# Optimization experiments

Hardware: AMD Instinct MI355X
Metric: run time of the kernel (lower is better)

## Reference

```python
import jax, jax.numpy as jnp
import numpy as np

D_MODEL = 1024
N_HEADS = 16
HEAD_DIM = D_MODEL // N_HEADS
B, S = 4, 2048


def setup_inputs() -> dict:
    key = jax.random.key(0)
    ks = jax.random.split(key, 12)
    s = 1.0 / np.sqrt(D_MODEL)
    inp = {
        'query': jax.random.normal(ks[0], (B, S, D_MODEL), jnp.float32),
        'key': jax.random.normal(ks[1], (B, S, D_MODEL), jnp.float32),
        'value': jax.random.normal(ks[2], (B, S, D_MODEL), jnp.float32),
        # causal mask, broadcast over batch and heads: [1,1,S,S]
        'mask': jnp.tril(jnp.ones((S, S), jnp.int32))[None, None],
        'Wq': jax.random.normal(ks[3], (D_MODEL, D_MODEL), jnp.float32) * s,
        'bq': jnp.zeros((D_MODEL,), jnp.float32),
        'Wk': jax.random.normal(ks[4], (D_MODEL, D_MODEL), jnp.float32) * s,
        'bk': jnp.zeros((D_MODEL,), jnp.float32),
        'Wv': jax.random.normal(ks[5], (D_MODEL, D_MODEL), jnp.float32) * s,
        'bv': jnp.zeros((D_MODEL,), jnp.float32),
        'Wo': jax.random.normal(ks[6], (D_MODEL, D_MODEL), jnp.float32) * s,
        'bo': jnp.zeros((D_MODEL,), jnp.float32),
    }
    return inp


def reference(query, key, value, mask, Wq, bq, Wk, bk, Wv, bv, Wo, bo):
    b, q_len, _ = query.shape
    scale = jnp.sqrt(jnp.float32(HEAD_DIM))
    # projections
    q = query @ Wq + bq
    k = key @ Wk + bk
    v = value @ Wv + bv
    # [b, h, s, hd]
    q = q.reshape(b, q_len, N_HEADS, HEAD_DIM).transpose(0, 2, 1, 3)
    k = k.reshape(b, -1, N_HEADS, HEAD_DIM).transpose(0, 2, 1, 3)
    v = v.reshape(b, -1, N_HEADS, HEAD_DIM).transpose(0, 2, 1, 3)
    scores = jnp.einsum('bhqd,bhkd->bhqk', q, k) / scale
    scores = jnp.where(mask == 0, jnp.float32(-jnp.inf), scores)
    attn = jax.nn.softmax(scores, axis=-1)  # dropout p=0 / eval mode
    out = jnp.einsum('bhqk,bhkd->bhqd', attn, v)
    out = out.transpose(0, 2, 1, 3).reshape(b, q_len, D_MODEL)
    return out @ Wo + bo
```

## Files before the change

### kernel.cpp

```cpp
#include <hip/hip_runtime.h>
#include <hip/hip_bf16.h>

typedef __attribute__((ext_vector_type(8))) short short8;
typedef __attribute__((ext_vector_type(4))) float floatx4;
typedef __attribute__((ext_vector_type(4))) unsigned short ushort4v;

#define D_MODEL 1024
#define S_LEN   2048
#define N_HEADS 16
#define HEAD_DIM 64
#define BATCH   4

__device__ __forceinline__ unsigned short f2bf(float x) {
    union { float f; unsigned int u; } v; v.f = x;
    unsigned int u = v.u;
    unsigned int r = (u + 0x7FFFu + ((u >> 16) & 1u)) >> 16;
    return (unsigned short)r;
}
__device__ __forceinline__ unsigned short f2bf_trunc(float x) {
    union { float f; unsigned int u; } v; v.f = x;
    return (unsigned short)(v.u >> 16);
}

__device__ __forceinline__ void gload_lds16(const void* g, void* s) {
    __builtin_amdgcn_global_load_lds(
        (const __attribute__((address_space(1))) void*)g,
        (__attribute__((address_space(3))) void*)s, 16, 0, 0);
}

struct Conv3 {
    const float* src[3];
    unsigned short* dst[3];
};

__global__ __launch_bounds__(256) void conv_bf16(Conv3 a) {
    const float* s = a.src[blockIdx.z];
    unsigned short* d = a.dst[blockIdx.z];
    size_t i = ((size_t)blockIdx.x * 256 + threadIdx.x) * 8;
    float4 f0 = *(const float4*)(s + i);
    float4 f1 = *(const float4*)(s + i + 4);
    short8 v;
    v[0] = (short)f2bf(f0.x); v[1] = (short)f2bf(f0.y);
    v[2] = (short)f2bf(f0.z); v[3] = (short)f2bf(f0.w);
    v[4] = (short)f2bf(f1.x); v[5] = (short)f2bf(f1.y);
    v[6] = (short)f2bf(f1.z); v[7] = (short)f2bf(f1.w);
    *(short8*)(d + i) = v;
}

struct Trans4 {
    const float* W[4];
    unsigned short* Wt[4];
};

__global__ __launch_bounds__(256) void transpose_w(Trans4 args) {
    __shared__ unsigned short tile[32][33];
    const float* W = args.W[blockIdx.z];
    unsigned short* Wt = args.Wt[blockIdx.z];
    int n0 = blockIdx.x * 32;
    int k0 = blockIdx.y * 32;
    int t = threadIdx.x;
    int r = t >> 5, c = t & 31;
    for (int i = 0; i < 4; ++i) {
        int k = k0 + r + i * 8;
        tile[r + i * 8][c] = f2bf(W[(size_t)k * D_MODEL + n0 + c]);
    }
    __syncthreads();
    for (int i = 0; i < 4; ++i) {
        int n = n0 + r + i * 8;
        Wt[(size_t)n * D_MODEL + k0 + c] = tile[c][r + i * 8];
    }
}

struct GemmIn {
    const unsigned short* A;
    const unsigned short* Bt;
    const float* bias;
    void* C;
    int mode;
    float scale;
};
struct Gemm3 { GemmIn g[3]; };

#define BAR()   asm volatile("s_barrier" ::: "memory")
#define LGKM0() asm volatile("s_waitcnt lgkmcnt(0)" ::: "memory")
#define VMW2()  asm volatile("s_waitcnt vmcnt(2)" ::: "memory")
#define VMW0()  asm volatile("s_waitcnt vmcnt(0)" ::: "memory")

#define READ_A4(BUF)                                                           \
    _Pragma("unroll") for (int ii = 0; ii < 4; ++ii) {                         \
        aF[ii][0] = *(const short8*)&lds[(BUF)*16384 + aOff + ii*512];         \
        aF[ii][1] = *(const short8*)&lds[(BUF)*16384 + aOff + ii*512 + 4096];  \
    }
#define READ_B4(BUF)                                                           \
    _Pragma("unroll") for (int jj = 0; jj < 4; ++jj) {                         \
        bF[jj][0] = *(const short8*)&lds[(BUF)*16384 + bOff + jj*512];         \
        bF[jj][1] = *(const short8*)&lds[(BUF)*16384 + bOff + jj*512 + 4096];  \
    }
#define MFMA_ALL()                                                             \
    __builtin_amdgcn_s_setprio(1);                                             \
    _Pragma("unroll") for (int ii = 0; ii < 4; ++ii)                           \
    _Pragma("unroll") for (int jj = 0; jj < 4; ++jj) {                         \
        acc[ii][jj] = __builtin_amdgcn_mfma_f32_16x16x32_bf16(                 \
            aF[ii][0], bF[jj][0], acc[ii][jj], 0, 0, 0);                       \
        acc[ii][jj] = __builtin_amdgcn_mfma_f32_16x16x32_bf16(                 \
            aF[ii][1], bF[jj][1], acc[ii][jj], 0, 0, 0);                       \
    }                                                                          \
    __builtin_amdgcn_s_setprio(0)

__global__ __launch_bounds__(256, 2) void gemm_128(Gemm3 args) {
    constexpr int K = D_MODEL, N = D_MODEL;
    constexpr int NT = K / 64;
    GemmIn g = args.g[blockIdx.z];

    __shared__ __align__(16) unsigned short lds[32768];

    const int m0 = blockIdx.x * 128;
    const int n0 = blockIdx.y * 128;
    const int t = threadIdx.x;
    const int w = t >> 6, lane = t & 63;
    const int quad = lane >> 4, l16 = lane & 15;
    const int wm = w >> 1, wn = w & 1;

    const int srow = w * 32 + (lane >> 2);
    const int scol = ((lane & 3) * 8) ^ ((lane & 32) ? 16 : 0);

    const int fx = (quad * 8) ^ ((l16 & 8) ? 16 : 0);
    const int aOff = (wm * 64 + l16) * 32 + fx;
    const int bOff = 8192 + (wn * 64 + l16) * 32 + fx;

    floatx4 acc[4][4] = {};
    short8 aF[4][2], bF[4][2];

    auto stageA = [&](int buf, int kt) {
        const unsigned short* s0 = g.A + (size_t)(m0 + srow) * K + kt * 64 + scol;
        unsigned short* d0 = &lds[buf * 16384 + (w * 32) * 32];
        gload_lds16(s0, d0);
        gload_lds16(s0 + 32, d0 + 4096);
        gload_lds16(s0 + (size_t)16 * K, d0 + 512);
        gload_lds16(s0 + (size_t)16 * K + 32, d0 + 512 + 4096);
    };
    auto stageB = [&](int buf, int kt) {
        const unsigned short* s0 = g.Bt + (size_t)(n0 + srow) * K + kt * 64 + scol;
        unsigned short* d0 = &lds[buf * 16384 + 8192 + (w * 32) * 32];
        gload_lds16(s0, d0);
        gload_lds16(s0 + 32, d0 + 4096);
        gload_lds16(s0 + (size_t)16 * K, d0 + 512);
        gload_lds16(s0 + (size_t)16 * K + 32, d0 + 512 + 4096);
    };

    stageA(0, 0); stageB(0, 0);
    VMW0();
    BAR();

#pragma unroll 2
    for (int kt = 0; kt < NT; ++kt) {
        const int buf = kt & 1;
        if (kt + 1 < NT) { stageA(buf ^ 1, kt + 1); stageB(buf ^ 1, kt + 1); }
        READ_A4(buf); READ_B4(buf);
        LGKM0();
        MFMA_ALL();
        if (kt + 1 < NT) { VMW0(); BAR(); }
    }

    if (g.mode == 2) {
        unsigned short* Ct = (unsigned short*)g.C;
#pragma unroll
        for (int j = 0; j < 4; ++j) {
            int col = n0 + wn * 64 + j * 16 + l16;
            int h = col >> 6, dd = col & 63;
            float bv = g.bias[col];
#pragma unroll
            for (int i = 0; i < 4; ++i) {
                int row0 = m0 + wm * 64 + i * 16 + quad * 4;
                int bb = row0 >> 11, s = row0 & 2047;
                ushort4v u;
#pragma unroll
                for (int r = 0; r < 4; ++r) u[r] = f2bf((acc[i][j][r] + bv) * g.scale);
                *(ushort4v*)(Ct + ((size_t)(bb * 16 + h) * 64 + dd) * 2048 + s) = u;
            }
        }
    } else {
#pragma unroll
        for (int j = 0; j < 4; ++j) {
            int col = n0 + wn * 64 + j * 16 + l16;
            float bv = g.bias[col];
#pragma unroll
            for (int i = 0; i < 4; ++i) {
#pragma unroll
                for (int r = 0; r < 4; ++r) {
                    int row = m0 + wm * 64 + i * 16 + quad * 4 + r;
                    float v = (acc[i][j][r] + bv) * g.scale;
                    if (g.mode == 1)
                        ((float*)g.C)[(size_t)row * N + col] = v;
                    else
                        ((unsigned short*)g.C)[(size_t)row * N + col] = f2bf(v);
                }
            }
        }
    }
}

__global__ __launch_bounds__(512) void flash_attn(
    const unsigned short* __restrict__ Qp,
    const unsigned short* __restrict__ Kp,
    const unsigned short* __restrict__ Vtg,
    unsigned short* __restrict__ Op) {
    constexpr int S = S_LEN, D = D_MODEL;
    __shared__ __align__(16) unsigned short Ks[2 * 4096];
    __shared__ __align__(16) unsigned short Vs[2 * 4096];
    __shared__ __align__(16) unsigned short Ps[8][1024];

    int id = blockIdx.x + (blockIdx.y << 3);
    int pair = (id >> 3) & 7;
    int bh = (id & 7) | ((id >> 6) << 3);
    int b = bh >> 4;
    int t = threadIdx.x;
    int wave = t >> 6, lane = t & 63;
    int quad = lane >> 4, l16 = lane & 15;

    const size_t head_off = (size_t)b * S * D + (size_t)(bh & 15) * HEAD_DIM;
    const unsigned short* Khead = Kp + head_off;
    const unsigned short* Vhead = Vtg + (size_t)bh * 64 * S;

    int q0l = pair * 128, q0h = (15 - pair) * 128;
    int qgl = q0l + wave * 16 + l16;
    int qgh = q0h + wave * 16 + l16;

    const unsigned short* qpl = Qp + head_off + (size_t)qgl * D + quad * 8;
    short8 ql0 = *(const short8*)qpl, ql1 = *(const short8*)(qpl + 32);
    const unsigned short* qph = Qp + head_off + (size_t)qgh * D + quad * 8;
    short8 qh0 = *(const short8*)qph, qh1 = *(const short8*)(qph + 32);

    floatx4 ol[4] = {}, oh[4] = {};
    floatx4 lsl = {}, lsh = {};

    short8 a1;
#pragma unroll
    for (int e = 0; e < 8; ++e) a1[e] = (l16 == 0) ? (short)0x3F80 : (short)0;

    int sw = wave & 3;
    bool doK = wave < 4;
    int srow = sw * 16 + (lane >> 2);
    int scol = ((lane & 3) * 8) ^ ((lane & 32) ? 16 : 0);

    auto stage = [&](int buf, int k0) {
        if (doK) {
            const unsigned short* s0 = Khead + (size_t)(k0 + srow) * D + scol;
            unsigned short* d0 = Ks + buf * 4096 + sw * 512;
            gload_lds16(s0, d0);
            gload_lds16(s0 + 32, d0 + 2048);
        } else {
            const unsigned short* s0 = Vhead + (size_t)srow * S + k0 + scol;
            unsigned short* d0 = Vs + buf * 4096 + sw * 512;
            gload_lds16(s0, d0);
            gload_lds16(s0 + 32, d0 + 2048);
        }
    };

    int wqminl = q0l + wave * 16, wqmaxl = wqminl + 15;
    int wqminh = q0h + wave * 16, wqmaxh = wqminh + 15;

    const int swz = (quad * 8) ^ ((l16 & 8) ? 16 : 0);
    const int pswz = (l16 & 8) ? 16 : 0;
    unsigned short* pw = &Ps[wave][0];

    auto half_step = [&](const unsigned short* Kb, const unsigned short* Vb,
                         int k0, int qg, int wqmin, floatx4& ls,
                         floatx4* o, short8 qb0, short8 qb1) {
        floatx4 st[4];
        __builtin_amdgcn_s_setprio(1);
        for (int gk = 0; gk < 4; ++gk) {
            short8 ka0 = *(const short8*)&Kb[(gk * 16 + l16) * 32 + swz];
            short8 ka1 = *(const short8*)&Kb[2048 + (gk * 16 + l16) * 32 + swz];
            floatx4 s = {};
            s = __builtin_amdgcn_mfma_f32_16x16x32_bf16(ka0, qb0, s, 0, 0, 0);
            s = __builtin_amdgcn_mfma_f32_16x16x32_bf16(ka1, qb1, s, 0, 0, 0);
            st[gk] = s;
        }
        __builtin_amdgcn_s_setprio(0);

        float sv[16];
        if (k0 + 63 < wqmin) {
            for (int i = 0; i < 16; ++i)
                sv[i] = __builtin_amdgcn_exp2f(st[i >> 2][i & 3]);
        } else {
            for (int gk = 0; gk < 4; ++gk)
                for (int r = 0; r < 4; ++r) {
                    int key = k0 + gk * 16 + quad * 4 + r;
                    sv[gk * 4 + r] = (key <= qg)
                        ? __builtin_amdgcn_exp2f(st[gk][r]) : 0.f;
                }
        }

        for (int gk = 0; gk < 4; ++gk) {
            ushort4v u;
            for (int r = 0; r < 4; ++r) u[r] = f2bf_trunc(sv[gk * 4 + r]);
            *(ushort4v*)&pw[(gk >> 1) * 512 + l16 * 32 +
                            ((((gk & 1) * 16) + quad * 4) ^ pswz)] = u;
        }

        short8 pf0 = *(const short8*)&pw[l16 * 32 + swz];
        short8 pf1 = *(const short8*)&pw[512 + l16 * 32 + swz];
        __builtin_amdgcn_s_setprio(1);
        ls = __builtin_amdgcn_mfma_f32_16x16x32_bf16(a1, pf0, ls, 0, 0, 0);
        ls = __builtin_amdgcn_mfma_f32_16x16x32_bf16(a1, pf1, ls, 0, 0, 0);
        for (int jd = 0; jd < 4; ++jd) {
            short8 va0 = *(const short8*)&Vb[(jd * 16 + l16) * 32 + swz];
            short8 va1 = *(const short8*)&Vb[2048 + (jd * 16 + l16) * 32 + swz];
            o[jd] = __builtin_amdgcn_mfma_f32_16x16x32_bf16(va0, pf0, o[jd], 0, 0, 0);
            o[jd] = __builtin_amdgcn_mfma_f32_16x16x32_bf16(va1, pf1, o[jd], 0, 0, 0);
        }
        __builtin_amdgcn_s_setprio(0);
    };

    int n_kt = 2 * (15 - pair) + 2;
    stage(0, 0);
    for (int kt = 0; kt < n_kt; ++kt) {
        int k0 = kt * 64;
        if (kt + 1 < n_kt) {
            stage((kt + 1) & 1, k0 + 64);
            VMW2();
        } else {
            VMW0();
        }
        BAR();

        const unsigned short* Kb = Ks + (kt & 1) * 4096;
        const unsigned short* Vb = Vs + (kt & 1) * 4096;
        if (k0 <= wqmaxl) half_step(Kb, Vb, k0, qgl, wqminl, lsl, ol, ql0, ql1);
        if (k0 <= wqmaxh) half_step(Kb, Vb, k0, qgh, wqminh, lsh, oh, qh0, qh1);
        BAR();
    }

    {
        float inv = 1.0f / __shfl(lsl[0], l16);
        unsigned short* op = Op + head_off + (size_t)qgl * D;
        for (int jd = 0; jd < 4; ++jd) {
            ushort4v u;
            for (int r = 0; r < 4; ++r) u[r] = f2bf(ol[jd][r] * inv);
            *(ushort4v*)(op + jd * 16 + quad * 4) = u;
        }
    }
    {
        float inv = 1.0f / __shfl(lsh[0], l16);
        unsigned short* op = Op + head_off + (size_t)qgh * D;
        for (int jd = 0; jd < 4; ++jd) {
            ushort4v u;
            for (int r = 0; r < 4; ++r) u[r] = f2bf(oh[jd][r] * inv);
            *(ushort4v*)(op + jd * 16 + quad * 4) = u;
        }
    }
}

extern "C" void kernel_launch(void* const* d_in, const int* in_sizes, int n_in,
                              void* d_out, int out_size, void* d_ws,
                              size_t ws_size, hipStream_t stream) {
    const float* query = (const float*)d_in[0];
    const float* key   = (const float*)d_in[1];
    const float* value = (const float*)d_in[2];
    const float* Wq = (const float*)d_in[4];
    const float* bq = (const float*)d_in[5];
    const float* Wk = (const float*)d_in[6];
    const float* bk = (const float*)d_in[7];
    const float* Wv = (const float*)d_in[8];
    const float* bv = (const float*)d_in[9];
    const float* Wo = (const float*)d_in[10];
    const float* bo = (const float*)d_in[11];
    float* out = (float*)d_out;

    char* ws = (char*)d_ws;
    const size_t WT_SZ = (size_t)D_MODEL * D_MODEL * 2;
    const size_t X_SZ = (size_t)BATCH * S_LEN * D_MODEL * 2;
    unsigned short* wtq = (unsigned short*)(ws);
    unsigned short* wtk = (unsigned short*)(ws + WT_SZ);
    unsigned short* wtv = (unsigned short*)(ws + 2 * WT_SZ);
    unsigned short* wto = (unsigned short*)(ws + 3 * WT_SZ);
    unsigned short* Qbf = (unsigned short*)(ws + 4 * WT_SZ);
    unsigned short* Kbf = (unsigned short*)(ws + 4 * WT_SZ + X_SZ);
    unsigned short* Vbf = (unsigned short*)(ws + 4 * WT_SZ + 2 * X_SZ);
    unsigned short* Qp  = (unsigned short*)(ws + 4 * WT_SZ + 3 * X_SZ);
    unsigned short* Kp  = (unsigned short*)(ws + 4 * WT_SZ + 4 * X_SZ);
    unsigned short* Vtg = (unsigned short*)(ws + 4 * WT_SZ + 5 * X_SZ);
    unsigned short* Ao  = Qbf;

    Trans4 ta;
    ta.W[0] = Wq; ta.W[1] = Wk; ta.W[2] = Wv; ta.W[3] = Wo;
    ta.Wt[0] = wtq; ta.Wt[1] = wtk; ta.Wt[2] = wtv; ta.Wt[3] = wto;
    transpose_w<<<dim3(32, 32, 4), 256, 0, stream>>>(ta);

    Conv3 ca;
    ca.src[0] = query; ca.src[1] = key; ca.src[2] = value;
    ca.dst[0] = Qbf;   ca.dst[1] = Kbf; ca.dst[2] = Vbf;
    conv_bf16<<<dim3(4096, 1, 3), 256, 0, stream>>>(ca);

    const float q_scale = 0.125f * 1.44269504088896340736f;
    Gemm3 gq;
    gq.g[0].A = Qbf; gq.g[0].Bt = wtq; gq.g[0].bias = bq; gq.g[0].C = Qp;  gq.g[0].mode = 0; gq.g[0].scale = q_scale;
    gq.g[1].A = Kbf; gq.g[1].Bt = wtk; gq.g[1].bias = bk; gq.g[1].C = Kp;  gq.g[1].mode = 0; gq.g[1].scale = 1.0f;
    gq.g[2].A = Vbf; gq.g[2].Bt = wtv; gq.g[2].bias = bv; gq.g[2].C = Vtg; gq.g[2].mode = 2; gq.g[2].scale = 1.0f;
    gemm_128<<<dim3(64, 8, 3), 256, 0, stream>>>(gq);

    flash_attn<<<dim3(8, BATCH * N_HEADS), 512, 0, stream>>>(
        Qp, Kp, Vtg, Ao);

    Gemm3 go;
    go.g[0].A = Ao; go.g[0].Bt = wto; go.g[0].bias = bo; go.g[0].C = out; go.g[0].mode = 1; go.g[0].scale = 1.0f;
    gemm_128<<<dim3(64, 8, 1), 256, 0, stream>>>(go);
}
```

Baseline: 312.8 us.

## Enlarge projection GEMM tiles to 256x256 with 8 waves and interleaved prefetch

Replaces the 128x128, 4-wave GEMM with a 256x256, 8-wave kernel that double-buffers 64 KB of LDS and prefetches two K-steps ahead. LDS reads and MFMA quadrants are interleaved with the next tile's global-to-LDS loads, and vmcnt waits are partial instead of full. The goal is higher arithmetic intensity per byte loaded and better overlap of loads with MFMA. In exchange, fewer blocks are launched, which underfills the GPU for the single output projection. The kernel also runs at one block per CU and adds many barriers.

New measurement: 346.8 us. 10.9% more time.

```diff
diff --git a/kernel.cpp b/kernel.cpp
--- a/kernel.cpp
+++ b/kernel.cpp
@@ -83,83 +83,96 @@
 
 #define BAR()   asm volatile("s_barrier" ::: "memory")
 #define LGKM0() asm volatile("s_waitcnt lgkmcnt(0)" ::: "memory")
+#define VMW8()  asm volatile("s_waitcnt vmcnt(8)" ::: "memory")
 #define VMW2()  asm volatile("s_waitcnt vmcnt(2)" ::: "memory")
 #define VMW0()  asm volatile("s_waitcnt vmcnt(0)" ::: "memory")
 
-#define READ_A4(BUF)                                                           \
+#define RD_A(BUF, I0)                                                          \
     _Pragma("unroll") for (int ii = 0; ii < 4; ++ii) {                         \
-        aF[ii][0] = *(const short8*)&lds[(BUF)*16384 + aOff + ii*512];         \
-        aF[ii][1] = *(const short8*)&lds[(BUF)*16384 + aOff + ii*512 + 4096];  \
-    }
-#define READ_B4(BUF)                                                           \
-    _Pragma("unroll") for (int jj = 0; jj < 4; ++jj) {                         \
-        bF[jj][0] = *(const short8*)&lds[(BUF)*16384 + bOff + jj*512];         \
-        bF[jj][1] = *(const short8*)&lds[(BUF)*16384 + bOff + jj*512 + 4096];  \
-    }
-#define MFMA_ALL()                                                             \
+        aF[ii][0] = *(const short8*)&lds[(BUF)*32768 + aOff + ((I0)+ii)*512];  \
+        aF[ii][1] = *(const short8*)&lds[(BUF)*32768 + aOff + ((I0)+ii)*512 + 4096]; \
+    }
+#define RD_B(BUF, J0, DST)                                                     \
+    _Pragma("unroll") for (int jj = 0; jj < 2; ++jj) {                         \
+        DST[jj][0] = *(const short8*)&lds[(BUF)*32768 + bOff + ((J0)+jj)*512]; \
+        DST[jj][1] = *(const short8*)&lds[(BUF)*32768 + bOff + ((J0)+jj)*512 + 4096]; \
+    }
+#define MQ(I0, J0, B)                                                          \
     __builtin_amdgcn_s_setprio(1);                                             \
     _Pragma("unroll") for (int ii = 0; ii < 4; ++ii)                           \
-    _Pragma("unroll") for (int jj = 0; jj < 4; ++jj) {                         \
-        acc[ii][jj] = __builtin_amdgcn_mfma_f32_16x16x32_bf16(                 \
-            aF[ii][0], bF[jj][0], acc[ii][jj], 0, 0, 0);                       \
-        acc[ii][jj] = __builtin_amdgcn_mfma_f32_16x16x32_bf16(                 \
-            aF[ii][1], bF[jj][1], acc[ii][jj], 0, 0, 0);                       \
+    _Pragma("unroll") for (int jj = 0; jj < 2; ++jj) {                         \
+        acc[(I0)+ii][(J0)+jj] = __builtin_amdgcn_mfma_f32_16x16x32_bf16(       \
+            aF[ii][0], B[jj][0], acc[(I0)+ii][(J0)+jj], 0, 0, 0);              \
+        acc[(I0)+ii][(J0)+jj] = __builtin_amdgcn_mfma_f32_16x16x32_bf16(       \
+            aF[ii][1], B[jj][1], acc[(I0)+ii][(J0)+jj], 0, 0, 0);              \
     }                                                                          \
     __builtin_amdgcn_s_setprio(0)
 
-__global__ __launch_bounds__(256, 2) void gemm_128(Gemm3 args) {
+__global__ __launch_bounds__(512, 1) void gemm_256(Gemm3 args) {
     constexpr int K = D_MODEL, N = D_MODEL;
     constexpr int NT = K / 64;
     GemmIn g = args.g[blockIdx.z];
 
-    __shared__ __align__(16) unsigned short lds[32768];
-
-    const int m0 = blockIdx.x * 128;
-    const int n0 = blockIdx.y * 128;
+    __shared__ __align__(16) unsigned short lds[65536];
+
+    const int m0 = blockIdx.x * 256;
+    const int n0 = blockIdx.y * 256;
     const int t = threadIdx.x;
     const int w = t >> 6, lane = t & 63;
     const int quad = lane >> 4, l16 = lane & 15;
-    const int wm = w >> 1, wn = w & 1;
-
-    const int srow = w * 32 + (lane >> 2);
-    const int scol = ((lane & 3) * 8) ^ ((lane & 32) ? 16 : 0);
+    const int wm = w >> 2, wn = w & 3;
+
+    const int srow = t >> 2;
+    const int scol = ((t & 3) * 8) ^ ((t & 32) ? 16 : 0);
 
     const int fx = (quad * 8) ^ ((l16 & 8) ? 16 : 0);
-    const int aOff = (wm * 64 + l16) * 32 + fx;
-    const int bOff = 8192 + (wn * 64 + l16) * 32 + fx;
-
-    floatx4 acc[4][4] = {};
-    short8 aF[4][2], bF[4][2];
-
-    auto stageA = [&](int buf, int kt) {
-        const unsigned short* s0 = g.A + (size_t)(m0 + srow) * K + kt * 64 + scol;
-        unsigned short* d0 = &lds[buf * 16384 + (w * 32) * 32];
+    const int aOff = wm * 8192 + l16 * 32 + fx;
+    const int bOff = 16384 + (wn >> 1) * 8192 + ((wn & 1) * 64 + l16) * 32 + fx;
+
+    floatx4 acc[8][4] = {};
+    short8 aF[4][2], bE[2][2], bO[2][2];
+
+    auto stageA = [&](int buf, int h, int kt) {
+        const unsigned short* s0 =
+            g.A + (size_t)(m0 + h * 128 + srow) * K + kt * 64 + scol;
+        unsigned short* d0 = &lds[buf * 32768 + h * 8192 + w * 512];
         gload_lds16(s0, d0);
         gload_lds16(s0 + 32, d0 + 4096);
-        gload_lds16(s0 + (size_t)16 * K, d0 + 512);
-        gload_lds16(s0 + (size_t)16 * K + 32, d0 + 512 + 4096);
     };
-    auto stageB = [&](int buf, int kt) {
-        const unsigned short* s0 = g.Bt + (size_t)(n0 + srow) * K + kt * 64 + scol;
-        unsigned short* d0 = &lds[buf * 16384 + 8192 + (w * 32) * 32];
+    auto stageB = [&](int buf, int h, int kt) {
+        const unsigned short* s0 =
+            g.Bt + (size_t)(n0 + h * 128 + srow) * K + kt * 64 + scol;
+        unsigned short* d0 = &lds[buf * 32768 + 16384 + h * 8192 + w * 512];
         gload_lds16(s0, d0);
         gload_lds16(s0 + 32, d0 + 4096);
-        gload_lds16(s0 + (size_t)16 * K, d0 + 512);
-        gload_lds16(s0 + (size_t)16 * K + 32, d0 + 512 + 4096);
     };
 
-    stageA(0, 0); stageB(0, 0);
-    VMW0();
+    stageA(0, 0, 0); stageA(0, 1, 0); stageB(0, 0, 0); stageB(0, 1, 0);
+    stageA(1, 0, 1); stageA(1, 1, 1); stageB(1, 0, 1); stageB(1, 1, 1);
+    VMW8();
     BAR();
 
-#pragma unroll 2
     for (int kt = 0; kt < NT; ++kt) {
         const int buf = kt & 1;
-        if (kt + 1 < NT) { stageA(buf ^ 1, kt + 1); stageB(buf ^ 1, kt + 1); }
-        READ_A4(buf); READ_B4(buf);
-        LGKM0();
-        MFMA_ALL();
-        if (kt + 1 < NT) { VMW0(); BAR(); }
+        const bool pf = (kt + 2 < NT);
+        RD_A(buf, 0); RD_B(buf, 0, bE);
+        BAR(); LGKM0();
+        MQ(0, 0, bE);
+        BAR();
+        RD_B(buf, 2, bO);
+        BAR(); LGKM0();
+        MQ(0, 2, bO);
+        BAR();
+        RD_A(buf, 4);
+        if (pf) { stageB(buf, 0, kt + 2); stageB(buf, 1, kt + 2); }
+        BAR(); LGKM0();
+        MQ(4, 2, bO);
+        BAR();
+        if (pf) { stageA(buf, 0, kt + 2); stageA(buf, 1, kt + 2); }
+        BAR();
+        MQ(4, 0, bE);
+        if (kt <= NT - 3) { VMW8(); } else if (kt == NT - 2) { VMW0(); }
+        BAR();
     }
 
     if (g.mode == 2) {
@@ -170,8 +183,8 @@
             int h = col >> 6, dd = col & 63;
             float bv = g.bias[col];
 #pragma unroll
-            for (int i = 0; i < 4; ++i) {
-                int row0 = m0 + wm * 64 + i * 16 + quad * 4;
+            for (int i = 0; i < 8; ++i) {
+                int row0 = m0 + wm * 128 + i * 16 + quad * 4;
                 int bb = row0 >> 11, s = row0 & 2047;
                 ushort4v u;
 #pragma unroll
@@ -185,10 +198,10 @@
             int col = n0 + wn * 64 + j * 16 + l16;
             float bv = g.bias[col];
 #pragma unroll
-            for (int i = 0; i < 4; ++i) {
+            for (int i = 0; i < 8; ++i) {
 #pragma unroll
                 for (int r = 0; r < 4; ++r) {
-                    int row = m0 + wm * 64 + i * 16 + quad * 4 + r;
+                    int row = m0 + wm * 128 + i * 16 + quad * 4 + r;
                     float v = (acc[i][j][r] + bv) * g.scale;
                     if (g.mode == 1)
                         ((float*)g.C)[(size_t)row * N + col] = v;
@@ -398,12 +411,12 @@
     gq.g[0].A = Qbf; gq.g[0].Bt = wtq; gq.g[0].bias = bq; gq.g[0].C = Qp;  gq.g[0].mode = 0; gq.g[0].scale = q_scale;
     gq.g[1].A = Kbf; gq.g[1].Bt = wtk; gq.g[1].bias = bk; gq.g[1].C = Kp;  gq.g[1].mode = 0; gq.g[1].scale = 1.0f;
     gq.g[2].A = Vbf; gq.g[2].Bt = wtv; gq.g[2].bias = bv; gq.g[2].C = Vtg; gq.g[2].mode = 2; gq.g[2].scale = 1.0f;
-    gemm_128<<<dim3(64, 8, 3), 256, 0, stream>>>(gq);
+    gemm_256<<<dim3(32, 4, 3), 512, 0, stream>>>(gq);
 
     flash_attn<<<dim3(8, BATCH * N_HEADS), 512, 0, stream>>>(
         Qp, Kp, Vtg, Ao);
 
     Gemm3 go;
     go.g[0].A = Ao; go.g[0].Bt = wto; go.g[0].bias = bo; go.g[0].C = out; go.g[0].mode = 1; go.g[0].scale = 1.0f;
-    gemm_128<<<dim3(64, 8, 1), 256, 0, stream>>>(go);
-}
+    gemm_256<<<dim3(32, 4, 1), 512, 0, stream>>>(go);
+}
```
